# Performance work log

Measured on AMD Instinct MI355X. Metric: run time of the kernel, lower is better.

## Reference

```python
import jax, jax.numpy as jnp
import numpy as np

D_MODEL = 1024
NUM_HEADS = 16
D_IN = 1024

def setup_inputs() -> dict:
    key = jax.random.key(0)
    ks = jax.random.split(key, 5)
    scale = 1.0 / np.sqrt(D_IN)
    return {
        "in_features": jax.random.normal(ks[0], (4, 2048, D_IN), dtype=jnp.float32),
        "q_weight": jax.random.normal(ks[1], (D_MODEL, D_IN), dtype=jnp.float32) * scale,
        "k_weight": jax.random.normal(ks[2], (D_MODEL, D_IN), dtype=jnp.float32) * scale,
        "v_weight": jax.random.normal(ks[3], (D_MODEL, D_IN), dtype=jnp.float32) * scale,
        "o_weight": jax.random.normal(ks[4], (D_MODEL, D_MODEL), dtype=jnp.float32) * scale,
    }

def reference(in_features, q_weight, k_weight, v_weight, o_weight):
    batch, seq_len, _ = in_features.shape
    d_head = D_MODEL // NUM_HEADS
    # QKV projections (Linear with no bias: x @ W^T)
    q = jnp.einsum('bsi,di->bsd', in_features, q_weight)
    k = jnp.einsum('bsi,di->bsd', in_features, k_weight)
    v = jnp.einsum('bsi,di->bsd', in_features, v_weight)
    # split heads -> [b, h, s, d_head]
    q = q.reshape(batch, seq_len, NUM_HEADS, d_head).transpose(0, 2, 1, 3)
    k = k.reshape(batch, seq_len, NUM_HEADS, d_head).transpose(0, 2, 1, 3)
    v = v.reshape(batch, seq_len, NUM_HEADS, d_head).transpose(0, 2, 1, 3)
    # scaled dot-product attention (scale by per-head dim, as in SelfAttention)
    scores = jnp.einsum('bhqd,bhkd->bhqk', q, k) / jnp.sqrt(jnp.float32(d_head))
    probs = jax.nn.softmax(scores, axis=-1)
    ctx = jnp.einsum('bhqk,bhkd->bhqd', probs, v)
    # merge heads -> [b, s, d_model]
    ctx = ctx.transpose(0, 2, 1, 3).reshape(batch, seq_len, D_MODEL)
    # output projection
    return jnp.einsum('bsd,md->bsm', ctx, o_weight)
```

## Files before the change

kernel.cpp:

```cpp
#include <hip/hip_runtime.h>

typedef _Float16 half8 __attribute__((ext_vector_type(8)));
typedef _Float16 half4v __attribute__((ext_vector_type(4)));
typedef __fp16 fp16x2 __attribute__((ext_vector_type(2)));
typedef float f32x4 __attribute__((ext_vector_type(4)));
typedef float f32x16 __attribute__((ext_vector_type(16)));

__device__ __forceinline__ void gload_lds16(const _Float16* g, _Float16* l) {
    __builtin_amdgcn_global_load_lds(
        (const __attribute__((address_space(1))) void*)g,
        (__attribute__((address_space(3))) void*)l,
        16, 0, 0);
}

__global__ void cvt4_f32_f16(const float* __restrict__ s0, const float* __restrict__ s1,
                             const float* __restrict__ s2, const float* __restrict__ s3,
                             _Float16* __restrict__ dst) {
    int i = blockIdx.x * blockDim.x + threadIdx.x;
    int wsel = blockIdx.y;
    const float* src = (wsel == 0) ? s0 : (wsel == 1) ? s1 : (wsel == 2) ? s2 : s3;
    f32x4 v = ((const f32x4*)src)[i];
    half4v h;
    h[0] = (_Float16)v[0]; h[1] = (_Float16)v[1];
    h[2] = (_Float16)v[2]; h[3] = (_Float16)v[3];
    ((half4v*)(dst + (size_t)wsel * 1048576))[i] = h;
}

__global__ __launch_bounds__(256, 2)
void gemm_qkv(const float* __restrict__ X,
              const _Float16* __restrict__ Wbase,
              _Float16* __restrict__ outbase)
{
    __shared__ _Float16 As[2][4096];
    __shared__ _Float16 Bs[2][4096];

    const int tid  = threadIdx.x;
    const int lane = tid & 63;
    const int w    = tid >> 6;
    const int wr   = w >> 1, wc = w & 1;
    const int lr   = lane & 15, lg = lane >> 4;
    const int brow = blockIdx.x * 128;
    const int bcol = blockIdx.y * 128;
    const int mat  = blockIdx.z;

    const float*    Ap = X + (size_t)brow * 1024;
    const _Float16* Bp = Wbase + (size_t)mat * (1024u * 1024u) + (size_t)bcol * 1024;

    const int srw   = tid >> 2;
    const int sch   = tid & 3;
    const int bsoff = ((sch ^ (srw & 3)) << 3);
    const int aw0 = srw * 32 + ((sch ^ (srw & 3)) << 3);
    const int aw1 = (64 + srw) * 32 + ((sch ^ ((64 + srw) & 3)) << 3);

    auto stageB = [&](int buf, int kt) {
        gload_lds16(Bp + (size_t)srw * 1024 + kt * 32 + bsoff,        &Bs[buf][w * 512]);
        gload_lds16(Bp + (size_t)(64 + srw) * 1024 + kt * 32 + bsoff, &Bs[buf][2048 + w * 512]);
    };

    f32x4 pa0, pa1, pa2, pa3;
    auto loadA = [&](int kt) {
        const float* p0 = Ap + (size_t)srw * 1024 + kt * 32 + sch * 8;
        const float* p1 = Ap + (size_t)(64 + srw) * 1024 + kt * 32 + sch * 8;
        pa0 = *(const f32x4*)p0;  pa1 = *(const f32x4*)(p0 + 4);
        pa2 = *(const f32x4*)p1;  pa3 = *(const f32x4*)(p1 + 4);
    };
    auto writeA = [&](int buf) {
        half8 h0, h1;
#pragma unroll
        for (int e = 0; e < 4; ++e) {
            h0[e]     = (_Float16)pa0[e];
            h0[4 + e] = (_Float16)pa1[e];
            h1[e]     = (_Float16)pa2[e];
            h1[4 + e] = (_Float16)pa3[e];
        }
        *(half8*)&As[buf][aw0] = h0;
        *(half8*)&As[buf][aw1] = h1;
    };

    f32x4 acc[4][4] = {};
    const int swz = ((lg ^ (lr & 3)) << 3);

    loadA(0);
    stageB(0, 0);
    writeA(0);
    __syncthreads();

    for (int t = 0; t < 32; ++t) {
        const int cur = t & 1;
        if (t < 31) {
            loadA(t + 1);
            stageB(cur ^ 1, t + 1);
        }
        half8 af[4], bf[4];
#pragma unroll
        for (int mi = 0; mi < 4; ++mi)
            af[mi] = *(const half8*)&As[cur][(wr * 64 + mi * 16 + lr) * 32 + swz];
#pragma unroll
        for (int ni = 0; ni < 4; ++ni)
            bf[ni] = *(const half8*)&Bs[cur][(wc * 64 + ni * 16 + lr) * 32 + swz];
        __builtin_amdgcn_s_setprio(1);
#pragma unroll
        for (int mi = 0; mi < 4; ++mi)
#pragma unroll
            for (int ni = 0; ni < 4; ++ni)
                acc[mi][ni] = __builtin_amdgcn_mfma_f32_16x16x32_f16(af[mi], bf[ni], acc[mi][ni], 0, 0, 0);
        __builtin_amdgcn_s_setprio(0);
        if (t < 31) writeA(cur ^ 1);
        __syncthreads();
    }

    _Float16* outp = outbase + (size_t)mat * (8192u * 1024u);
    if (mat == 2) {
        _Float16* Ts = &As[0][0];
#pragma unroll
        for (int p = 0; p < 2; ++p) {
            __syncthreads();
            if (wc == p) {
#pragma unroll
                for (int mi = 0; mi < 4; ++mi)
#pragma unroll
                    for (int ni = 0; ni < 4; ++ni) {
                        int drow = ni * 16 + lr;
                        int s0   = wr * 64 + mi * 16 + lg * 4;
                        half4v o;
#pragma unroll
                        for (int r = 0; r < 4; ++r) o[r] = (_Float16)acc[mi][ni][r];
                        int byteoff = drow * 256 + s0 * 2;
                        byteoff ^= (drow & 7) << 4;
                        *(half4v*)((char*)Ts + byteoff) = o;
                    }
            }
            __syncthreads();
            {
                int row   = tid >> 2;
                int cbase = (tid & 3) * 4;
                int gd = bcol + p * 64 + row;
                int h = gd >> 6, dd = gd & 63;
                int b = brow >> 11, sseq = brow & 2047;
                _Float16* gout = outp + (((size_t)b * 16 + h) * 64 + dd) * 2048 + sseq;
#pragma unroll
                for (int j = 0; j < 4; ++j) {
                    int c  = cbase + j;
                    int lc = c ^ (row & 7);
                    half8 v = *(const half8*)&Ts[row * 128 + lc * 8];
                    *(half8*)&gout[c * 8] = v;
                }
            }
        }
    } else {
        const float scale = (mat == 0) ? 0.18033688f : 1.0f;
#pragma unroll
        for (int mi = 0; mi < 4; ++mi)
#pragma unroll
            for (int ni = 0; ni < 4; ++ni)
#pragma unroll
                for (int r = 0; r < 4; ++r) {
                    int row = brow + wr * 64 + mi * 16 + lg * 4 + r;
                    int col = bcol + wc * 64 + ni * 16 + lr;
                    int b = row >> 11, s = row & 2047;
                    int h = col >> 6,  d = col & 63;
                    outp[(((size_t)b * 16 + h) * 2048 + s) * 64 + d] =
                        (_Float16)(acc[mi][ni][r] * scale);
                }
    }
}

__global__ __launch_bounds__(256, 2)
void gemm_o(const _Float16* __restrict__ A,
            const _Float16* __restrict__ Wbase,
            float* __restrict__ outp)
{
    __shared__ _Float16 lds[32768];
    _Float16* Asb = lds;
    _Float16* Bsb = lds + 16384;

    const int tid  = threadIdx.x;
    const int lane = tid & 63;
    const int w    = tid >> 6;
    const int wr   = w >> 1, wc = w & 1;
    const int lr   = lane & 15, lg = lane >> 4;
    const int brow = blockIdx.x * 128;
    const int bcol = blockIdx.y * 128;

    const _Float16* Ap = A + (size_t)brow * 1024;
    const _Float16* Bp = Wbase + (size_t)bcol * 1024;

    const int srw  = tid >> 2;
    const int sch  = tid & 3;
    const int soff = ((sch ^ (srw & 3)) << 3);

    auto stage = [&](int buf, int kt) {
#pragma unroll
        for (int i = 0; i < 2; ++i) {
            const int ra = i * 64 + srw;
            gload_lds16(Ap + (size_t)ra * 1024 + kt * 32 + soff,
                        Asb + buf * 4096 + i * 2048 + w * 512);
            gload_lds16(Bp + (size_t)ra * 1024 + kt * 32 + soff,
                        Bsb + buf * 4096 + i * 2048 + w * 512);
        }
    };

    f32x4 acc[4][4] = {};
    const int swz = ((lg ^ (lr & 3)) << 3);

    stage(0, 0);
    stage(1, 1);
    asm volatile("s_waitcnt vmcnt(4)" ::: "memory");
    __builtin_amdgcn_s_barrier();
    __builtin_amdgcn_sched_barrier(0);

    for (int t = 0; t < 32; ++t) {
        if (t < 30) stage((t + 2) & 3, t + 2);
        const _Float16* Ab = Asb + (t & 3) * 4096;
        const _Float16* Bb = Bsb + (t & 3) * 4096;
        half8 af[4], bf[4];
#pragma unroll
        for (int mi = 0; mi < 4; ++mi)
            af[mi] = *(const half8*)&Ab[(wr * 64 + mi * 16 + lr) * 32 + swz];
#pragma unroll
        for (int ni = 0; ni < 4; ++ni)
            bf[ni] = *(const half8*)&Bb[(wc * 64 + ni * 16 + lr) * 32 + swz];
        __builtin_amdgcn_s_setprio(1);
#pragma unroll
        for (int mi = 0; mi < 4; ++mi)
#pragma unroll
            for (int ni = 0; ni < 4; ++ni)
                acc[mi][ni] = __builtin_amdgcn_mfma_f32_16x16x32_f16(af[mi], bf[ni], acc[mi][ni], 0, 0, 0);
        __builtin_amdgcn_s_setprio(0);
        if (t < 30)       { asm volatile("s_waitcnt vmcnt(4)" ::: "memory"); }
        else if (t == 30) { asm volatile("s_waitcnt vmcnt(0)" ::: "memory"); }
        if (t < 31) {
            __builtin_amdgcn_s_barrier();
            __builtin_amdgcn_sched_barrier(0);
        }
    }

#pragma unroll
    for (int mi = 0; mi < 4; ++mi)
#pragma unroll
        for (int ni = 0; ni < 4; ++ni)
#pragma unroll
            for (int r = 0; r < 4; ++r) {
                int row = brow + wr * 64 + mi * 16 + lg * 4 + r;
                int col = bcol + wc * 64 + ni * 16 + lr;
                outp[(size_t)row * 1024 + col] = acc[mi][ni][r];
            }
}

#define M_FIX 10.0f
__global__ __launch_bounds__(256, 2)
void attn_kernel(const _Float16* __restrict__ Q,
                 const _Float16* __restrict__ Kx,
                 const _Float16* __restrict__ Vt,
                 _Float16* __restrict__ Ctx)
{
    __shared__ _Float16 Ks[2][64 * 72];
    __shared__ _Float16 Vs[2][64 * 72];

    const int tid = threadIdx.x, lane = tid & 63, w = tid >> 6;
    const int l31 = lane & 31, hi = lane >> 5;

    const int wg = blockIdx.x;
    const int j = ((wg & 7) << 6) + (wg >> 3);
    const int bh = j >> 3, qblk = j & 7;

    const _Float16* Qp  = Q  + ((size_t)bh * 2048 + qblk * 256) * 64;
    const _Float16* Kp  = Kx + (size_t)bh * 2048 * 64;
    const _Float16* Vtp = Vt + (size_t)bh * 64 * 2048;

    half8 qf[2][4];
#pragma unroll
    for (int g = 0; g < 2; ++g)
#pragma unroll
        for (int ks = 0; ks < 4; ++ks)
            qf[g][ks] = *(const half8*)(Qp + (size_t)(w * 64 + g * 32 + l31) * 64 + ks * 16 + hi * 8);

    const int srow = tid >> 3;
    const int scol = (tid & 7) * 8;
    const _Float16* Kg0 = Kp  + (size_t)srow * 64   + scol;
    const _Float16* Vg0 = Vtp + (size_t)srow * 2048 + scol;
    const int ldso = srow * 72 + scol;

    const fp16x2 ones2 = {(__fp16)1.0f, (__fp16)1.0f};

    f32x16 cacc[2][2] = {};
    float lp[2][2] = {};

    half8 kr0, kr1, vr0, vr1;
    kr0 = *(const half8*)(Kg0);
    kr1 = *(const half8*)(Kg0 + 2048);
    vr0 = *(const half8*)(Vg0);
    vr1 = *(const half8*)(Vg0 + 32 * 2048);
    *(half8*)&Ks[0][ldso]           = kr0;
    *(half8*)&Ks[0][ldso + 32 * 72] = kr1;
    *(half8*)&Vs[0][ldso]           = vr0;
    *(half8*)&Vs[0][ldso + 32 * 72] = vr1;
    __syncthreads();

    for (int t = 0; t < 32; ++t) {
        const int cur = t & 1;
        if (t < 31) {
            kr0 = *(const half8*)(Kg0 + (size_t)(t + 1) * 4096);
            kr1 = *(const half8*)(Kg0 + (size_t)(t + 1) * 4096 + 2048);
        }

        f32x16 sf[2][2];
        __builtin_amdgcn_s_setprio(1);
#pragma unroll
        for (int g = 0; g < 2; ++g)
#pragma unroll
            for (int kt = 0; kt < 2; ++kt) {
                f32x16 z;
#pragma unroll
                for (int r = 0; r < 16; ++r) z[r] = -M_FIX;
#pragma unroll
                for (int ks = 0; ks < 4; ++ks) {
                    half8 kf = *(const half8*)&Ks[cur][(kt * 32 + l31) * 72 + ks * 16 + hi * 8];
                    z = __builtin_amdgcn_mfma_f32_32x32x16_f16(kf, qf[g][ks], z, 0, 0, 0);
                }
                sf[g][kt] = z;
            }
        __builtin_amdgcn_s_setprio(0);

        if (t < 31) {
            *(half8*)&Ks[cur ^ 1][ldso]           = kr0;
            *(half8*)&Ks[cur ^ 1][ldso + 32 * 72] = kr1;
            vr0 = *(const half8*)(Vg0 + (t + 1) * 64);
            vr1 = *(const half8*)(Vg0 + (t + 1) * 64 + 32 * 2048);
        }

#pragma unroll
        for (int g = 0; g < 2; ++g) {
            half8 bf[4];
#pragma unroll
            for (int kt = 0; kt < 2; ++kt) {
#pragma unroll
                for (int r = 0; r < 16; ++r)
                    sf[g][kt][r] = __builtin_amdgcn_exp2f(sf[g][kt][r]);

                unsigned uq[4][2];
#pragma unroll
                for (int qd = 0; qd < 4; ++qd)
#pragma unroll
                    for (int w2 = 0; w2 < 2; ++w2)
                        uq[qd][w2] = __builtin_bit_cast(unsigned,
                            __builtin_amdgcn_cvt_pkrtz(sf[g][kt][4 * qd + 2 * w2],
                                                       sf[g][kt][4 * qd + 2 * w2 + 1]));

#pragma unroll
                for (int k1 = 0; k1 < 2; ++k1) {
                    union { half8 h; unsigned u[4]; } bu;
#pragma unroll
                    for (int w2 = 0; w2 < 2; ++w2) {
                        unsigned a = uq[2 * k1][w2];
                        unsigned b = uq[2 * k1 + 1][w2];
                        asm("v_permlane32_swap_b32 %0, %1" : "+v"(a), "+v"(b));
                        bu.u[w2]     = a;
                        bu.u[2 + w2] = b;
                    }
                    lp[g][0] = __builtin_amdgcn_fdot2(__builtin_bit_cast(fp16x2, bu.u[0]), ones2, lp[g][0], false);
                    lp[g][1] = __builtin_amdgcn_fdot2(__builtin_bit_cast(fp16x2, bu.u[1]), ones2, lp[g][1], false);
                    lp[g][0] = __builtin_amdgcn_fdot2(__builtin_bit_cast(fp16x2, bu.u[2]), ones2, lp[g][0], false);
                    lp[g][1] = __builtin_amdgcn_fdot2(__builtin_bit_cast(fp16x2, bu.u[3]), ones2, lp[g][1], false);
                    bf[kt * 2 + k1] = bu.h;
                }
            }

            __builtin_amdgcn_s_setprio(1);
#pragma unroll
            for (int dt = 0; dt < 2; ++dt)
#pragma unroll
                for (int ks = 0; ks < 4; ++ks) {
                    half8 vf = *(const half8*)&Vs[cur][(dt * 32 + l31) * 72 + ks * 16 + hi * 8];
                    cacc[g][dt] = __builtin_amdgcn_mfma_f32_32x32x16_f16(vf, bf[ks], cacc[g][dt], 0, 0, 0);
                }
            __builtin_amdgcn_s_setprio(0);
        }

        if (t < 31) {
            *(half8*)&Vs[cur ^ 1][ldso]           = vr0;
            *(half8*)&Vs[cur ^ 1][ldso + 32 * 72] = vr1;
        }
        __syncthreads();
    }

#pragma unroll
    for (int g = 0; g < 2; ++g) {
        float l = lp[g][0] + lp[g][1];
        const float inv = 1.0f / (l + __shfl_xor(l, 32, 64));
        const int s = qblk * 256 + w * 64 + g * 32 + l31;
        _Float16* Cp = Ctx + ((size_t)(bh >> 4) * 2048 + s) * 1024 + (bh & 15) * 64;
#pragma unroll
        for (int dt = 0; dt < 2; ++dt)
#pragma unroll
            for (int qd = 0; qd < 4; ++qd) {
                half4v o;
#pragma unroll
                for (int j2 = 0; j2 < 4; ++j2) o[j2] = (_Float16)(cacc[g][dt][4 * qd + j2] * inv);
                *(half4v*)&Cp[dt * 32 + qd * 8 + hi * 4] = o;
            }
    }
}

extern "C" void kernel_launch(void* const* d_in, const int* in_sizes, int n_in,
                              void* d_out, int out_size, void* d_ws, size_t ws_size,
                              hipStream_t stream)
{
    const float* X  = (const float*)d_in[0];
    const float* Wq = (const float*)d_in[1];
    const float* Wk = (const float*)d_in[2];
    const float* Wv = (const float*)d_in[3];
    const float* Wo = (const float*)d_in[4];

    if (ws_size < (size_t)(8 + 4 + 24) * 1024 * 1024 * 2) return;
    _Float16* Ctx = (_Float16*)d_ws;
    _Float16* Wh  = Ctx + (size_t)8 * 1024 * 1024;
    _Float16* QKV = Wh + (size_t)4 * 1024 * 1024;

    cvt4_f32_f16<<<dim3(1024, 4), 256, 0, stream>>>(Wq, Wk, Wv, Wo, Wh);

    gemm_qkv<<<dim3(64, 8, 3), 256, 0, stream>>>(X, Wh, QKV);

    attn_kernel<<<512, 256, 0, stream>>>(QKV, QKV + 8388608, QKV + 16777216, Ctx);

    gemm_o<<<dim3(64, 8), 256, 0, stream>>>(Ctx, Wh + 3145728, (float*)d_out);
}
```

Before: 187.9 us.

## Deepen QKV GEMM pipeline to four LDS buffers and change swizzle pattern

Moves the QKV projection GEMM from double-buffered shared memory with __syncthreads to a four-slot ring with prefetch distance two. Completion is tracked with explicit vmcnt/lgkmcnt waits and raw s_barrier, mirroring the output GEMM. It also changes the LDS XOR swizzle in both GEMMs to use (row>>1)&3 so fragment reads hit fewer bank conflicts. The cost is twice the LDS per block, which may cut occupancy, plus more intricate wait-count bookkeeping.

```diff
diff --git a/kernel.cpp b/kernel.cpp
--- a/kernel.cpp
+++ b/kernel.cpp
@@ -31,8 +31,9 @@
               const _Float16* __restrict__ Wbase,
               _Float16* __restrict__ outbase)
 {
-    __shared__ _Float16 As[2][4096];
-    __shared__ _Float16 Bs[2][4096];
+    __shared__ _Float16 lds[32768];
+    _Float16* Asb = lds;
+    _Float16* Bsb = lds + 16384;
 
     const int tid  = threadIdx.x;
     const int lane = tid & 63;
@@ -46,15 +47,16 @@
     const float*    Ap = X + (size_t)brow * 1024;
     const _Float16* Bp = Wbase + (size_t)mat * (1024u * 1024u) + (size_t)bcol * 1024;
 
-    const int srw   = tid >> 2;
-    const int sch   = tid & 3;
-    const int bsoff = ((sch ^ (srw & 3)) << 3);
-    const int aw0 = srw * 32 + ((sch ^ (srw & 3)) << 3);
-    const int aw1 = (64 + srw) * 32 + ((sch ^ ((64 + srw) & 3)) << 3);
+    const int srw = tid >> 2;
+    const int sch = tid & 3;
+    const int rsw = (srw >> 1) & 3;
+    const int bso = ((sch ^ rsw) << 3);
+    const int aw0 = srw * 32        + ((sch ^ rsw) << 3);
+    const int aw1 = (64 + srw) * 32 + ((sch ^ rsw) << 3);
 
     auto stageB = [&](int buf, int kt) {
-        gload_lds16(Bp + (size_t)srw * 1024 + kt * 32 + bsoff,        &Bs[buf][w * 512]);
-        gload_lds16(Bp + (size_t)(64 + srw) * 1024 + kt * 32 + bsoff, &Bs[buf][2048 + w * 512]);
+        gload_lds16(Bp + (size_t)srw * 1024 + kt * 32 + bso,        Bsb + buf * 4096 + w * 512);
+        gload_lds16(Bp + (size_t)(64 + srw) * 1024 + kt * 32 + bso, Bsb + buf * 4096 + 2048 + w * 512);
     };
 
     f32x4 pa0, pa1, pa2, pa3;
@@ -73,31 +75,37 @@
             h1[e]     = (_Float16)pa2[e];
             h1[4 + e] = (_Float16)pa3[e];
         }
-        *(half8*)&As[buf][aw0] = h0;
-        *(half8*)&As[buf][aw1] = h1;
+        *(half8*)&Asb[buf * 4096 + aw0] = h0;
+        *(half8*)&Asb[buf * 4096 + aw1] = h1;
     };
 
     f32x4 acc[4][4] = {};
-    const int swz = ((lg ^ (lr & 3)) << 3);
+    const int swz = ((lg ^ ((lr >> 1) & 3)) << 3);
 
     loadA(0);
     stageB(0, 0);
     writeA(0);
-    __syncthreads();
+    loadA(1);
+    stageB(1, 1);
+    writeA(1);
+    asm volatile("s_waitcnt vmcnt(2) lgkmcnt(0)" ::: "memory");
+    __builtin_amdgcn_s_barrier();
+    __builtin_amdgcn_sched_barrier(0);
 
     for (int t = 0; t < 32; ++t) {
-        const int cur = t & 1;
-        if (t < 31) {
-            loadA(t + 1);
-            stageB(cur ^ 1, t + 1);
-        }
+        if (t < 30) {
+            loadA(t + 2);
+            stageB((t + 2) & 3, t + 2);
+        }
+        const _Float16* Ab = Asb + (t & 3) * 4096;
+        const _Float16* Bb = Bsb + (t & 3) * 4096;
         half8 af[4], bf[4];
 #pragma unroll
         for (int mi = 0; mi < 4; ++mi)
-            af[mi] = *(const half8*)&As[cur][(wr * 64 + mi * 16 + lr) * 32 + swz];
+            af[mi] = *(const half8*)&Ab[(wr * 64 + mi * 16 + lr) * 32 + swz];
 #pragma unroll
         for (int ni = 0; ni < 4; ++ni)
-            bf[ni] = *(const half8*)&Bs[cur][(wc * 64 + ni * 16 + lr) * 32 + swz];
+            bf[ni] = *(const half8*)&Bb[(wc * 64 + ni * 16 + lr) * 32 + swz];
         __builtin_amdgcn_s_setprio(1);
 #pragma unroll
         for (int mi = 0; mi < 4; ++mi)
@@ -105,13 +113,22 @@
             for (int ni = 0; ni < 4; ++ni)
                 acc[mi][ni] = __builtin_amdgcn_mfma_f32_16x16x32_f16(af[mi], bf[ni], acc[mi][ni], 0, 0, 0);
         __builtin_amdgcn_s_setprio(0);
-        if (t < 31) writeA(cur ^ 1);
-        __syncthreads();
+        if (t < 30) {
+            asm volatile("s_waitcnt vmcnt(2)" ::: "memory");
+            writeA((t + 2) & 3);
+        } else if (t == 30) {
+            asm volatile("s_waitcnt vmcnt(0)" ::: "memory");
+        }
+        if (t < 31) {
+            asm volatile("s_waitcnt lgkmcnt(0)" ::: "memory");
+            __builtin_amdgcn_s_barrier();
+            __builtin_amdgcn_sched_barrier(0);
+        }
     }
 
     _Float16* outp = outbase + (size_t)mat * (8192u * 1024u);
     if (mat == 2) {
-        _Float16* Ts = &As[0][0];
+        _Float16* Ts = lds;
 #pragma unroll
         for (int p = 0; p < 2; ++p) {
             __syncthreads();
@@ -187,7 +204,7 @@
 
     const int srw  = tid >> 2;
     const int sch  = tid & 3;
-    const int soff = ((sch ^ (srw & 3)) << 3);
+    const int soff = ((sch ^ ((srw >> 1) & 3)) << 3);
 
     auto stage = [&](int buf, int kt) {
 #pragma unroll
@@ -201,7 +218,7 @@
     };
 
     f32x4 acc[4][4] = {};
-    const int swz = ((lg ^ (lr & 3)) << 3);
+    const int swz = ((lg ^ ((lr >> 1) & 3)) << 3);
 
     stage(0, 0);
     stage(1, 1);
```

New measurement: 192.1 us. 2.2% more time.
